# Kernel optimization log

Hardware: AMD Instinct MI355X
Metric: run time of the kernel (lower is better)

## Reference

```python
import jax, jax.numpy as jnp
import numpy as np

BT, NV, NB, NS, H, W = 8, 10000, 16384, 4096, 256, 256


def setup_inputs() -> dict:
    key = jax.random.key(0)
    k1, k2, k3, k4 = jax.random.split(key, 4)
    verts = jax.random.normal(k1, (BT, NV, 3), dtype=jnp.float32)
    bds_v = jax.random.normal(k2, (BT, NB, 3), dtype=jnp.float32)
    # last channel of bds is a {0,1} mask over boundary samples
    bds_m = (jax.random.uniform(k3, (BT, NB, 1)) > 0.5).astype(jnp.float32)
    bds = jnp.concatenate([bds_v, bds_m], axis=-1)  # [bt, nb, 4]
    pix_to_face = jnp.zeros((BT, H, W, 1), dtype=jnp.int32)  # only shape is used upstream
    # deterministic replacement for torch.randperm(nb)[:n_samples]
    indices = jax.random.permutation(k4, NB)[:NS].astype(jnp.int64)
    return {"verts": verts, "bds": bds, "pix_to_face": pix_to_face, "indices": indices}


def reference(verts, bds, pix_to_face, indices):
    # sample boundary points and mask
    bds_v = bds[:, indices, :-1]          # [bt, ns, 3]
    bds_m = bds[:, indices, -1]           # [bt, ns]
    # squared euclidean distances (= torch.cdist(...)**2): [bt, ns, nv]
    sq_b = jnp.sum(bds_v * bds_v, axis=-1)              # [bt, ns]
    sq_v = jnp.sum(verts * verts, axis=-1)              # [bt, nv]
    cross = jnp.einsum('bsd,bvd->bsv', bds_v, verts)    # [bt, ns, nv]
    dist = sq_b[:, :, None] + sq_v[:, None, :] - 2.0 * cross
    # topk(k=1, largest=False) == min over verts
    min_dists = jnp.min(dist, axis=-1)                   # [bt, ns]
    # (min_dists * mask).mean over k (=1) and samples, then over batch (reduce=True)
    loss = jnp.mean(min_dists * bds_m, axis=-1)          # [bt]
    return jnp.mean(loss)
```

## Files before the change

### kernel.cpp

```cpp
#include <hip/hip_runtime.h>
#include <float.h>

#define BT 8
#define NV 10000
#define NB 16384
#define NS 4096
#define NPTS (BT * NS)
#define PTSB 2048
#define PB (NPTS / PTSB)
#define VCH 32
#define CH 313
#define SVMAX 316

__device__ __forceinline__ float min3f(float a, float b, float c) {
    float d;
    asm("v_min3_f32 %0, %1, %2, %3" : "=v"(d) : "v"(a), "v"(b), "v"(c));
    return d;
}

__global__ void __launch_bounds__(256, 4)
stage1(const float* __restrict__ verts, const float4* __restrict__ bds4,
       const int* __restrict__ idx, float* __restrict__ pmin) {
    __shared__ float4 sv[SVMAX];
    const int tid = threadIdx.x;
    const int pb  = blockIdx.x & (PB - 1);
    const int c   = blockIdx.x >> 4;
    const int b   = pb >> 1;
    const int p0  = pb * PTSB;
    const int v0  = c * CH;
    const int vend = (v0 + CH < NV) ? (v0 + CH) : NV;
    const int tn  = vend - v0;
    const int tn4 = (tn + 3) & ~3;

    for (int i = tid; i < tn4; i += 256) {
        float4 q;
        if (i < tn) {
            const float* vp = verts + (size_t)(b * NV + v0 + i) * 3;
            float x = vp[0], y = vp[1], z = vp[2];
            q = make_float4(-2.0f * x, -2.0f * y, -2.0f * z, x * x + y * y + z * z);
        } else {
            q = make_float4(0.0f, 0.0f, 0.0f, 3.4e38f);
        }
        sv[i] = q;
    }

    float bx[8], by[8], bz[8], m[8];
#pragma unroll
    for (int k = 0; k < 8; ++k) {
        int pt = p0 + tid + k * 256;
        float4 bp = bds4[(size_t)b * NB + idx[pt & (NS - 1)]];
        bx[k] = bp.x; by[k] = bp.y; bz[k] = bp.z;
        m[k] = FLT_MAX;
    }
    __syncthreads();

    for (int v = 0; v < tn4; v += 4) {
        float4 q0 = sv[v], q1 = sv[v + 1], q2 = sv[v + 2], q3 = sv[v + 3];
#pragma unroll
        for (int k = 0; k < 8; ++k) {
            float t0 = fmaf(bx[k], q0.x, fmaf(by[k], q0.y, fmaf(bz[k], q0.z, q0.w)));
            float t1 = fmaf(bx[k], q1.x, fmaf(by[k], q1.y, fmaf(bz[k], q1.z, q1.w)));
            float t2 = fmaf(bx[k], q2.x, fmaf(by[k], q2.y, fmaf(bz[k], q2.z, q2.w)));
            float t3 = fmaf(bx[k], q3.x, fmaf(by[k], q3.y, fmaf(bz[k], q3.z, q3.w)));
            m[k] = min3f(m[k], t0, t1);
            m[k] = min3f(m[k], t2, t3);
        }
    }

#pragma unroll
    for (int k = 0; k < 8; ++k)
        pmin[(size_t)c * NPTS + p0 + tid + k * 256] = m[k];
}

__global__ void stage2(const float* __restrict__ pmin, const float4* __restrict__ bds4,
                       const int* __restrict__ idx, float* __restrict__ bsum) {
    int pt = blockIdx.x * 256 + threadIdx.x;
    int b = pt >> 12, s = pt & (NS - 1);
    float4 bp = bds4[(size_t)b * NB + idx[s]];
    float md = FLT_MAX;
#pragma unroll 8
    for (int c = 0; c < VCH; ++c)
        md = fminf(md, pmin[(size_t)c * NPTS + pt]);
    float sqb = bp.x * bp.x + bp.y * bp.y + bp.z * bp.z;
    float val = (md + sqb) * bp.w * (1.0f / (float)NPTS);
    for (int o = 32; o > 0; o >>= 1) val += __shfl_down(val, o, 64);
    __shared__ float red[4];
    if ((threadIdx.x & 63) == 0) red[threadIdx.x >> 6] = val;
    __syncthreads();
    if (threadIdx.x == 0) bsum[blockIdx.x] = red[0] + red[1] + red[2] + red[3];
}

__global__ void stage3(const float* __restrict__ bsum, float* __restrict__ out) {
    float v = bsum[threadIdx.x];
    for (int o = 32; o > 0; o >>= 1) v += __shfl_down(v, o, 64);
    __shared__ float r[2];
    if ((threadIdx.x & 63) == 0) r[threadIdx.x >> 6] = v;
    __syncthreads();
    if (threadIdx.x == 0) out[0] = r[0] + r[1];
}

extern "C" void kernel_launch(void* const* d_in, const int* in_sizes, int n_in,
                              void* d_out, int out_size, void* d_ws, size_t ws_size,
                              hipStream_t stream) {
    const float*  verts = (const float*)d_in[0];
    const float4* bds4  = (const float4*)d_in[1];
    const int*    idx   = (const int*)d_in[3];
    float* out = (float*)d_out;

    char* ws = (char*)d_ws;
    float* pmin = (float*)ws;
    float* bsum = (float*)(ws + (size_t)VCH * NPTS * sizeof(float));

    stage1<<<PB * VCH, 256, 0, stream>>>(verts, bds4, idx, pmin);
    stage2<<<NPTS / 256, 256, 0, stream>>>(pmin, bds4, idx, bsum);
    stage3<<<1, 128, 0, stream>>>(bsum, out);
}
```

Before: 45.11 us.

## Retile stage1 to whole-batch points per block with smaller vertex chunks

Each stage1 block now covers all 4096 samples of one batch, 16 per thread, against an 80-vertex chunk. This gives 125 vertex chunks and 1000 blocks, where before there were 32 chunks and 512 blocks. The padding and tail handling go away because 80 divides 10000 evenly, and each shared-memory vertex read is reused across twice as many points. In exchange, register pressure per thread doubles, the partial-min buffer grows about fourfold, and stage2 has more global reads to reduce.

```diff
diff --git a/kernel.cpp b/kernel.cpp
--- a/kernel.cpp
+++ b/kernel.cpp
@@ -6,11 +6,9 @@
 #define NB 16384
 #define NS 4096
 #define NPTS (BT * NS)
-#define PTSB 2048
-#define PB (NPTS / PTSB)
-#define VCH 32
-#define CH 313
-#define SVMAX 316
+#define VCH 125
+#define CH 80
+#define PB 8
 
 __device__ __forceinline__ float min3f(float a, float b, float c) {
     float d;
@@ -21,43 +19,33 @@
 __global__ void __launch_bounds__(256, 4)
 stage1(const float* __restrict__ verts, const float4* __restrict__ bds4,
        const int* __restrict__ idx, float* __restrict__ pmin) {
-    __shared__ float4 sv[SVMAX];
+    __shared__ float4 sv[CH];
     const int tid = threadIdx.x;
-    const int pb  = blockIdx.x & (PB - 1);
-    const int c   = blockIdx.x >> 4;
-    const int b   = pb >> 1;
-    const int p0  = pb * PTSB;
+    const int b   = blockIdx.x & (PB - 1);
+    const int c   = blockIdx.x >> 3;
     const int v0  = c * CH;
-    const int vend = (v0 + CH < NV) ? (v0 + CH) : NV;
-    const int tn  = vend - v0;
-    const int tn4 = (tn + 3) & ~3;
 
-    for (int i = tid; i < tn4; i += 256) {
-        float4 q;
-        if (i < tn) {
-            const float* vp = verts + (size_t)(b * NV + v0 + i) * 3;
-            float x = vp[0], y = vp[1], z = vp[2];
-            q = make_float4(-2.0f * x, -2.0f * y, -2.0f * z, x * x + y * y + z * z);
-        } else {
-            q = make_float4(0.0f, 0.0f, 0.0f, 3.4e38f);
-        }
-        sv[i] = q;
+    if (tid < CH) {
+        const float* vp = verts + (size_t)(b * NV + v0 + tid) * 3;
+        float x = vp[0], y = vp[1], z = vp[2];
+        sv[tid] = make_float4(-2.0f * x, -2.0f * y, -2.0f * z,
+                              x * x + y * y + z * z);
     }
 
-    float bx[8], by[8], bz[8], m[8];
+    float bx[16], by[16], bz[16], m[16];
 #pragma unroll
-    for (int k = 0; k < 8; ++k) {
-        int pt = p0 + tid + k * 256;
-        float4 bp = bds4[(size_t)b * NB + idx[pt & (NS - 1)]];
+    for (int k = 0; k < 16; ++k) {
+        int s = tid + k * 256;
+        float4 bp = bds4[(size_t)b * NB + idx[s]];
         bx[k] = bp.x; by[k] = bp.y; bz[k] = bp.z;
         m[k] = FLT_MAX;
     }
     __syncthreads();
 
-    for (int v = 0; v < tn4; v += 4) {
+    for (int v = 0; v < CH; v += 4) {
         float4 q0 = sv[v], q1 = sv[v + 1], q2 = sv[v + 2], q3 = sv[v + 3];
 #pragma unroll
-        for (int k = 0; k < 8; ++k) {
+        for (int k = 0; k < 16; ++k) {
             float t0 = fmaf(bx[k], q0.x, fmaf(by[k], q0.y, fmaf(bz[k], q0.z, q0.w)));
             float t1 = fmaf(bx[k], q1.x, fmaf(by[k], q1.y, fmaf(bz[k], q1.z, q1.w)));
             float t2 = fmaf(bx[k], q2.x, fmaf(by[k], q2.y, fmaf(bz[k], q2.z, q2.w)));
@@ -68,8 +56,8 @@
     }
 
 #pragma unroll
-    for (int k = 0; k < 8; ++k)
-        pmin[(size_t)c * NPTS + p0 + tid + k * 256] = m[k];
+    for (int k = 0; k < 16; ++k)
+        pmin[(size_t)c * NPTS + b * NS + tid + k * 256] = m[k];
 }
 
 __global__ void stage2(const float* __restrict__ pmin, const float4* __restrict__ bds4,
@@ -78,7 +66,7 @@
     int b = pt >> 12, s = pt & (NS - 1);
     float4 bp = bds4[(size_t)b * NB + idx[s]];
     float md = FLT_MAX;
-#pragma unroll 8
+#pragma unroll 5
     for (int c = 0; c < VCH; ++c)
         md = fminf(md, pmin[(size_t)c * NPTS + pt]);
     float sqb = bp.x * bp.x + bp.y * bp.y + bp.z * bp.z;
```

New measurement: 65.25 us. +44.6%, slower.

## Split vertices into more chunks and merge partial minima with atomicMin

Applied to the files above, without the earlier changes.

Doubles the vertex-chunk count to 64 so the main kernel launches 1024 blocks instead of 512, which improves occupancy across CUs. Each block now folds its per-point minima into a single global array with atomicMin on order-preserving encoded floats. This replaces the 32-way partial-min buffer and the two reduction kernels. A prep kernel gathers the sampled boundary points once and initialises the min buffer, and a single 1024-thread finalize kernel does a deterministic fixed-point sum. The cost is atomic traffic, an extra launch, and a one-block serial final reduction.

```diff
diff --git a/kernel.cpp b/kernel.cpp
--- a/kernel.cpp
+++ b/kernel.cpp
@@ -6,49 +6,64 @@
 #define NB 16384
 #define NS 4096
 #define NPTS (BT * NS)
-#define PTSB 2048
-#define PB (NPTS / PTSB)
-#define VCH 32
-#define CH 313
-#define SVMAX 316
+#define PB 16
+#define VCH 64
+#define CH 157
+#define CHPAD 160
 
 __device__ __forceinline__ float min3f(float a, float b, float c) {
     float d;
     asm("v_min3_f32 %0, %1, %2, %3" : "=v"(d) : "v"(a), "v"(b), "v"(c));
     return d;
 }
+__device__ __forceinline__ unsigned enc(float f) {
+    unsigned u = __float_as_uint(f);
+    return (u & 0x80000000u) ? ~u : (u | 0x80000000u);
+}
+__device__ __forceinline__ float dec(unsigned u) {
+    unsigned v = (u & 0x80000000u) ? (u & 0x7FFFFFFFu) : ~u;
+    return __uint_as_float(v);
+}
+
+__global__ void prep(const float4* __restrict__ bds4, const int* __restrict__ idx,
+                     float4* __restrict__ bg, unsigned* __restrict__ pmin) {
+    int pt = blockIdx.x * 256 + threadIdx.x;
+    int b = pt >> 12, s = pt & (NS - 1);
+    bg[pt] = bds4[(size_t)b * NB + idx[s]];
+    pmin[pt] = 0xFFFFFFFFu;
+}
 
 __global__ void __launch_bounds__(256, 4)
-stage1(const float* __restrict__ verts, const float4* __restrict__ bds4,
-       const int* __restrict__ idx, float* __restrict__ pmin) {
-    __shared__ float4 sv[SVMAX];
+mainker(const float* __restrict__ verts, const float4* __restrict__ bg,
+        unsigned* __restrict__ pmin) {
+    __shared__ float4 sv[CHPAD];
     const int tid = threadIdx.x;
     const int pb  = blockIdx.x & (PB - 1);
     const int c   = blockIdx.x >> 4;
     const int b   = pb >> 1;
-    const int p0  = pb * PTSB;
+    const int p0  = pb * 2048;
     const int v0  = c * CH;
     const int vend = (v0 + CH < NV) ? (v0 + CH) : NV;
     const int tn  = vend - v0;
     const int tn4 = (tn + 3) & ~3;
 
-    for (int i = tid; i < tn4; i += 256) {
+    if (tid < tn4) {
         float4 q;
-        if (i < tn) {
-            const float* vp = verts + (size_t)(b * NV + v0 + i) * 3;
+        if (tid < tn) {
+            const float* vp = verts + (size_t)(b * NV + v0 + tid) * 3;
             float x = vp[0], y = vp[1], z = vp[2];
-            q = make_float4(-2.0f * x, -2.0f * y, -2.0f * z, x * x + y * y + z * z);
+            q = make_float4(-2.0f * x, -2.0f * y, -2.0f * z,
+                            x * x + y * y + z * z);
         } else {
             q = make_float4(0.0f, 0.0f, 0.0f, 3.4e38f);
         }
-        sv[i] = q;
+        sv[tid] = q;
     }
 
     float bx[8], by[8], bz[8], m[8];
 #pragma unroll
     for (int k = 0; k < 8; ++k) {
-        int pt = p0 + tid + k * 256;
-        float4 bp = bds4[(size_t)b * NB + idx[pt & (NS - 1)]];
+        float4 bp = bg[p0 + tid + k * 256];
         bx[k] = bp.x; by[k] = bp.y; bz[k] = bp.z;
         m[k] = FLT_MAX;
     }
@@ -69,34 +84,30 @@
 
 #pragma unroll
     for (int k = 0; k < 8; ++k)
-        pmin[(size_t)c * NPTS + p0 + tid + k * 256] = m[k];
+        atomicMin(&pmin[p0 + tid + k * 256], enc(m[k]));
 }
 
-__global__ void stage2(const float* __restrict__ pmin, const float4* __restrict__ bds4,
-                       const int* __restrict__ idx, float* __restrict__ bsum) {
-    int pt = blockIdx.x * 256 + threadIdx.x;
-    int b = pt >> 12, s = pt & (NS - 1);
-    float4 bp = bds4[(size_t)b * NB + idx[s]];
-    float md = FLT_MAX;
-#pragma unroll 8
-    for (int c = 0; c < VCH; ++c)
-        md = fminf(md, pmin[(size_t)c * NPTS + pt]);
-    float sqb = bp.x * bp.x + bp.y * bp.y + bp.z * bp.z;
-    float val = (md + sqb) * bp.w * (1.0f / (float)NPTS);
-    for (int o = 32; o > 0; o >>= 1) val += __shfl_down(val, o, 64);
-    __shared__ float red[4];
-    if ((threadIdx.x & 63) == 0) red[threadIdx.x >> 6] = val;
+__global__ void __launch_bounds__(1024)
+finalize(const unsigned* __restrict__ pmin, const float4* __restrict__ bg,
+         float* __restrict__ out) {
+    __shared__ long long sl[1024];
+    const int tid = threadIdx.x;
+    long long acc = 0;
+    for (int i = tid; i < NPTS; i += 1024) {
+        float md = dec(pmin[i]);
+        float4 bp = bg[i];
+        float sqb = bp.x * bp.x + bp.y * bp.y + bp.z * bp.z;
+        float val = (md + sqb) * bp.w;
+        acc += llrint((double)val * 1099511627776.0);
+    }
+    sl[tid] = acc;
     __syncthreads();
-    if (threadIdx.x == 0) bsum[blockIdx.x] = red[0] + red[1] + red[2] + red[3];
-}
-
-__global__ void stage3(const float* __restrict__ bsum, float* __restrict__ out) {
-    float v = bsum[threadIdx.x];
-    for (int o = 32; o > 0; o >>= 1) v += __shfl_down(v, o, 64);
-    __shared__ float r[2];
-    if ((threadIdx.x & 63) == 0) r[threadIdx.x >> 6] = v;
-    __syncthreads();
-    if (threadIdx.x == 0) out[0] = r[0] + r[1];
+    for (int o = 512; o > 0; o >>= 1) {
+        if (tid < o) sl[tid] += sl[tid + o];
+        __syncthreads();
+    }
+    if (tid == 0)
+        out[0] = (float)((double)sl[0] / 1099511627776.0 / (double)NPTS);
 }
 
 extern "C" void kernel_launch(void* const* d_in, const int* in_sizes, int n_in,
@@ -108,10 +119,10 @@
     float* out = (float*)d_out;
 
     char* ws = (char*)d_ws;
-    float* pmin = (float*)ws;
-    float* bsum = (float*)(ws + (size_t)VCH * NPTS * sizeof(float));
+    float4*   bg   = (float4*)ws;
+    unsigned* pmin = (unsigned*)(ws + (size_t)NPTS * sizeof(float4));
 
-    stage1<<<PB * VCH, 256, 0, stream>>>(verts, bds4, idx, pmin);
-    stage2<<<NPTS / 256, 256, 0, stream>>>(pmin, bds4, idx, bsum);
-    stage3<<<1, 128, 0, stream>>>(bsum, out);
+    prep<<<NPTS / 256, 256, 0, stream>>>(bds4, idx, bg, pmin);
+    mainker<<<PB * VCH, 256, 0, stream>>>(verts, bg, pmin);
+    finalize<<<1, 1024, 0, stream>>>(pmin, bg, out);
 }
```

New measurement: 48.30 us. 7.1% more time.
